# Optimization experiments

Hardware: AMD Instinct MI355X
Metric: run time of the kernel (lower is better)

The kernel has to match this reference:

```python
import jax, jax.numpy as jnp
import numpy as np

BETA = 0.25
N_E = 256
E_DIM = 1024


def setup_inputs() -> dict:
    key = jax.random.key(0)
    k1, k2, k3, k4 = jax.random.split(key, 4)
    z = jax.random.normal(k1, (16, E_DIM, 32, 32), dtype=jnp.float32)
    emb = jax.random.normal(k2, (N_E, E_DIM), dtype=jnp.float32)
    conv_w = jax.random.normal(k3, (E_DIM, E_DIM), dtype=jnp.float32) * 0.02
    conv_b = jax.random.normal(k4, (E_DIM,), dtype=jnp.float32) * 0.02
    return {"z": z, "emb": emb, "conv_w": conv_w, "conv_b": conv_b}


def reference(z, emb, conv_w, conv_b):
    # z: [B, C=e_dim, H, W] -> channels-last, flatten spatial+batch
    zp = jnp.transpose(z, (0, 2, 3, 1))          # [B, H, W, C]
    zf = zp.reshape(-1, E_DIM)                    # [N, C]
    # squared L2 distances to codebook: [N, n_e]
    d = (jnp.sum(zf * zf, axis=1, keepdims=True)
         + jnp.sum(emb * emb, axis=1)
         - 2.0 * (zf @ emb.T))
    min_idx = jnp.argmin(d, axis=1)               # [N]
    min_enc = jax.nn.one_hot(min_idx, N_E, dtype=z.dtype)  # [N, n_e]
    z_q = (min_enc @ emb).reshape(zp.shape)       # gather via matmul, as original
    # VQ commitment loss with straight-through estimator
    loss = (jnp.mean((jax.lax.stop_gradient(z_q) - zp) ** 2)
            + BETA * jnp.mean((z_q - jax.lax.stop_gradient(zp)) ** 2))
    z_q = zp + jax.lax.stop_gradient(z_q - zp)
    e_mean = jnp.mean(min_enc, axis=0)
    perplexity = jnp.exp(-jnp.sum(e_mean * jnp.log(e_mean + 1e-10)))
    # back to channels-first, then 1x1 conv (= per-pixel GEMM)
    z_q = jnp.transpose(z_q, (0, 3, 1, 2))        # [B, C, H, W]
    out = jnp.einsum('bchw,oc->bohw', z_q, conv_w) + conv_b[None, :, None, None]
    return out, loss, perplexity, min_idx
```

## Files before the change

### kernel.cpp

```cpp
#include <hip/hip_runtime.h>
#include <math.h>

#define NE 256
#define EDIM 1024
#define HW 1024
#define NPIX 16384
#define OUT_ELEMS 16777216

typedef short short8 __attribute__((ext_vector_type(8)));
typedef float f32x4 __attribute__((ext_vector_type(4)));

#define WS_HIST   0
#define WS_LOSS   1024
#define WS_ZSQ    1028
#define WS_NFLAG  1032
#define WS_T      4096
#define WS_MEMSET 1052672
#define WS_CE2    1052672
#define WS_FLAG   1053696
#define WS_IDX    1119232
#define WS_EH     1184768
#define WS_NEED   1709056

#define MAXF 16384
#define DELTA 0.6f

#define WO_CE2  0
#define WO_HIST 1024
#define WO_LOSS 2048
#define WO_IDX  4096
#define WO_T    69632
#define WO_TOTAL 1118208

__device__ __forceinline__ unsigned short f2bf(float f) {
    unsigned u = __float_as_uint(f);
    unsigned r = u + 0x7FFFu + ((u >> 16) & 1u);
    return (unsigned short)(r >> 16);
}

__device__ __forceinline__ void stage16(const void* g, void* l) {
    __builtin_amdgcn_global_load_lds(
        (const __attribute__((address_space(1))) unsigned int*)g,
        (__attribute__((address_space(3))) unsigned int*)l, 16, 0, 0);
}

__global__ __launch_bounds__(64) void k_prep(const float* __restrict__ emb,
                                             unsigned short* __restrict__ eh,
                                             float* __restrict__ ce2) {
    int j = blockIdx.x;
    int l = threadIdx.x;
    const float* row = emb + ((size_t)j << 10);
    float s = 0.f;
    #pragma unroll
    for (int i = 0; i < 4; i++) {
        float4 v = *(const float4*)(row + l * 4 + 256 * i);
        s += v.x * v.x + v.y * v.y + v.z * v.z + v.w * v.w;
        uint2 hp;
        hp.x = (unsigned)f2bf(v.x) | ((unsigned)f2bf(v.y) << 16);
        hp.y = (unsigned)f2bf(v.z) | ((unsigned)f2bf(v.w) << 16);
        *(uint2*)(eh + ((size_t)j << 10) + l * 4 + 256 * i) = hp;
    }
    #pragma unroll
    for (int m = 32; m; m >>= 1) s += __shfl_down(s, m, 64);
    if (l == 0) ce2[j] = 0.5f * s;
}

__global__ __launch_bounds__(256) void k_wT(const float* __restrict__ w,
                                            const float* __restrict__ emb,
                                            float* __restrict__ T) {
    __shared__ float wt[64 * 17];
    __shared__ float et[64 * 17];
    int t = threadIdx.x;
    int j0 = blockIdx.x * 64;
    int o0 = blockIdx.y * 64;
    int kb = blockIdx.z * 256;
    int to = t & 15, tj = t >> 4;
    float acc[4][4] = {};
    int lr = t >> 2, lk = (t & 3) * 4;
    for (int kk = kb; kk < kb + 256; kk += 16) {
        float4 wv = *(const float4*)(w + (size_t)(o0 + lr) * EDIM + kk + lk);
        float4 ev = *(const float4*)(emb + (size_t)(j0 + lr) * EDIM + kk + lk);
        __syncthreads();
        wt[lr * 17 + lk + 0] = wv.x; wt[lr * 17 + lk + 1] = wv.y;
        wt[lr * 17 + lk + 2] = wv.z; wt[lr * 17 + lk + 3] = wv.w;
        et[lr * 17 + lk + 0] = ev.x; et[lr * 17 + lk + 1] = ev.y;
        et[lr * 17 + lk + 2] = ev.z; et[lr * 17 + lk + 3] = ev.w;
        __syncthreads();
        #pragma unroll
        for (int k = 0; k < 16; k++) {
            float a[4], b[4];
            #pragma unroll
            for (int i = 0; i < 4; i++) a[i] = wt[(to * 4 + i) * 17 + k];
            #pragma unroll
            for (int i = 0; i < 4; i++) b[i] = et[(tj * 4 + i) * 17 + k];
            #pragma unroll
            for (int i = 0; i < 4; i++)
                #pragma unroll
                for (int jx = 0; jx < 4; jx++) acc[i][jx] += a[i] * b[jx];
        }
    }
    #pragma unroll
    for (int i = 0; i < 4; i++)
        #pragma unroll
        for (int jx = 0; jx < 4; jx++)
            atomicAdd(&T[(size_t)(o0 + to * 4 + i) * NE + j0 + tj * 4 + jx],
                      acc[i][jx]);
}

__global__ __launch_bounds__(256) void k_dist(
        const float* __restrict__ z, const unsigned short* __restrict__ eh,
        const float* __restrict__ ce2,
        int* __restrict__ idx_i, float* __restrict__ idx_f,
        int* __restrict__ hist, float* __restrict__ loss_s,
        float* __restrict__ zsq_acc,
        int* __restrict__ nflag, int* __restrict__ flagged) {
    __shared__ unsigned short sB[2][256 * 32];
    int t = threadIdx.x;
    int lane = t & 63, w = t >> 6;
    int m = lane & 15, quad = lane >> 4;
    int px0 = blockIdx.x * 64;
    int b = px0 >> 10;
    const float* zp = z + (((size_t)b) << 20) + (px0 & 1023) + w * 16 + m;
    int sc = t >> 2, so = (t & 3) * 8;

    f32x4 acc[16];
    #pragma unroll
    for (int nt = 0; nt < 16; nt++) acc[nt] = (f32x4){0.f, 0.f, 0.f, 0.f};

    #pragma unroll
    for (int i = 0; i < 4; i++)
        stage16(eh + (((size_t)(i * 64 + sc)) << 10) + so,
                &sB[0][(i * 256 + w * 64) * 8]);
    float zv[8];
    #pragma unroll
    for (int j = 0; j < 8; j++)
        zv[j] = zp[((size_t)(quad * 8 + j)) << 10];

    float zsq = 0.f;
    for (int ck = 0; ck < 32; ck++) {
        int cur = ck & 1;
        __syncthreads();
        short8 af;
        #pragma unroll
        for (int j = 0; j < 8; j++) {
            zsq += zv[j] * zv[j];
            ((unsigned short*)&af)[j] = f2bf(zv[j]);
        }
        if (ck < 31) {
            int kk = (ck + 1) * 32;
            #pragma unroll
            for (int i = 0; i < 4; i++)
                stage16(eh + (((size_t)(i * 64 + sc)) << 10) + kk + so,
                        &sB[1 - cur][(i * 256 + w * 64) * 8]);
            #pragma unroll
            for (int j = 0; j < 8; j++)
                zv[j] = zp[((size_t)(kk + quad * 8 + j)) << 10];
        }
        #pragma unroll
        for (int nt = 0; nt < 16; nt++) {
            short8 bf = *(const short8*)&sB[cur][(nt * 16 + m) * 32 + quad * 8];
            acc[nt] = __builtin_amdgcn_mfma_f32_16x16x32_bf16(af, bf, acc[nt], 0, 0, 0);
        }
    }

    #pragma unroll
    for (int msk = 32; msk; msk >>= 1) zsq += __shfl_down(zsq, msk, 64);
    if (lane == 0) atomicAdd(zsq_acc, zsq);

    float c2v[16];
    #pragma unroll
    for (int nt = 0; nt < 16; nt++) c2v[nt] = ce2[nt * 16 + m];

    float lsum = 0.f;
    #pragma unroll
    for (int r = 0; r < 4; r++) {
        float v1 = 3.4e38f, v2 = 3.4e38f; int i1 = 0;
        #pragma unroll
        for (int nt = 0; nt < 16; nt++) {
            int code = nt * 16 + m;
            float sv = c2v[nt] - acc[nt][r];
            if (sv < v1 || (sv == v1 && code < i1)) { v2 = v1; v1 = sv; i1 = code; }
            else v2 = fminf(v2, sv);
        }
        #pragma unroll
        for (int msk = 1; msk < 16; msk <<= 1) {
            float ov1 = __shfl_xor(v1, msk, 64);
            int   oi1 = __shfl_xor(i1, msk, 64);
            float ov2 = __shfl_xor(v2, msk, 64);
            float nv2 = fminf(fminf(v2, ov2), fmaxf(v1, ov1));
            if (ov1 < v1 || (ov1 == v1 && oi1 < i1)) { v1 = ov1; i1 = oi1; }
            v2 = nv2;
        }
        if (m == 0) {
            int px = px0 + w * 16 + quad * 4 + r;
            idx_i[px] = i1;
            idx_f[px] = (float)i1;
            atomicAdd(&hist[i1], 1);
            if (v2 - v1 < DELTA) {
                int pos = atomicAdd(nflag, 1);
                if (pos < MAXF) flagged[pos] = px;
            }
            lsum += v1;
        }
    }
    lsum += __shfl_xor(lsum, 16, 64);
    lsum += __shfl_xor(lsum, 32, 64);
    if (lane == 0) atomicAdd(loss_s, lsum);
}

__global__ __launch_bounds__(256) void k_cleanup(const float* __restrict__ z,
        const float* __restrict__ emb, const float* __restrict__ ce2,
        const int* __restrict__ nflag, const int* __restrict__ flagged,
        int* __restrict__ idx_i, float* __restrict__ idx_f, int* __restrict__ hist) {
    __shared__ float zs[1024];
    __shared__ float rv[4];
    __shared__ int ri[4];
    int t = threadIdx.x;
    int nf = *nflag; if (nf > MAXF) nf = MAXF;
    const float* er = emb + (size_t)t * EDIM;
    for (int i = blockIdx.x; i < nf; i += gridDim.x) {
        int px = flagged[i];
        int b = px >> 10, p = px & 1023;
        const float* zb = z + (((size_t)b) << 20) + p;
        #pragma unroll
        for (int r = 0; r < 4; r++) {
            int c = t + 256 * r;
            zs[c] = zb[((size_t)c) << 10];
        }
        __syncthreads();
        float d0 = 0.f, d1 = 0.f, d2 = 0.f, d3 = 0.f;
        #pragma unroll 4
        for (int c = 0; c < EDIM; c += 16) {
            float4 e0 = *(const float4*)(er + c);
            float4 e1 = *(const float4*)(er + c + 4);
            float4 e2 = *(const float4*)(er + c + 8);
            float4 e3 = *(const float4*)(er + c + 12);
            d0 += e0.x * zs[c]      + e0.y * zs[c + 1]  + e0.z * zs[c + 2]  + e0.w * zs[c + 3];
            d1 += e1.x * zs[c + 4]  + e1.y * zs[c + 5]  + e1.z * zs[c + 6]  + e1.w * zs[c + 7];
            d2 += e2.x * zs[c + 8]  + e2.y * zs[c + 9]  + e2.z * zs[c + 10] + e2.w * zs[c + 11];
            d3 += e3.x * zs[c + 12] + e3.y * zs[c + 13] + e3.z * zs[c + 14] + e3.w * zs[c + 15];
        }
        float sv = ce2[t] - ((d0 + d1) + (d2 + d3));
        int bi = t;
        #pragma unroll
        for (int msk = 1; msk < 64; msk <<= 1) {
            float ov = __shfl_xor(sv, msk, 64);
            int oi = __shfl_xor(bi, msk, 64);
            if (ov < sv || (ov == sv && oi < bi)) { sv = ov; bi = oi; }
        }
        if ((t & 63) == 0) { rv[t >> 6] = sv; ri[t >> 6] = bi; }
        __syncthreads();
        if (t == 0) {
            float v = rv[0]; int ix = ri[0];
            for (int ww = 1; ww < 4; ww++)
                if (rv[ww] < v || (rv[ww] == v && ri[ww] < ix)) { v = rv[ww]; ix = ri[ww]; }
            int old = idx_i[px];
            if (ix != old) {
                idx_i[px] = ix; idx_f[px] = (float)ix;
                atomicAdd(&hist[ix], 1); atomicSub(&hist[old], 1);
            }
        }
        __syncthreads();
    }
}

__global__ __launch_bounds__(64) void k_norms(const float* __restrict__ emb,
                                              float* __restrict__ ce2) {
    int j = blockIdx.x;
    int lane = threadIdx.x;
    const float* row = emb + (size_t)j * EDIM;
    float s = 0.f;
    #pragma unroll
    for (int i = 0; i < EDIM / 64; i++) {
        float v = row[lane + 64 * i];
        s += v * v;
    }
    #pragma unroll
    for (int m = 32; m; m >>= 1) s += __shfl_down(s, m, 64);
    if (lane == 0) ce2[j] = 0.5f * s;
}

__global__ __launch_bounds__(256) void k_argmin(const float* __restrict__ z,
                                                const float* __restrict__ emb,
                                                const float* __restrict__ ce2,
                                                int* __restrict__ idx_i,
                                                float* __restrict__ idx_f,
                                                int* __restrict__ hist,
                                                float* __restrict__ loss_acc) {
    __shared__ float zt[32 * 64];
    __shared__ float et[256 * 34];
    __shared__ float znorm_s[64];
    int t = threadIdx.x;
    int n0 = blockIdx.x * 64;
    int b = n0 >> 10;
    int p0 = n0 & 1023;
    const float* zb = z + (size_t)b * EDIM * HW;
    int tc = t & 31, tp = t >> 5;
    float acc[8][8] = {};
    float znorm = 0.f;
    for (int kk = 0; kk < EDIM; kk += 32) {
        #pragma unroll
        for (int i = 0; i < 16; i++) {
            int q = t + 256 * i;
            int code = q >> 4, k2 = q & 15;
            float2 v = *(const float2*)(emb + (size_t)code * EDIM + kk + k2 * 2);
            *(float2*)(et + code * 34 + k2 * 2) = v;
        }
        #pragma unroll
        for (int i = 0; i < 4; i++) {
            int q = t + 256 * i;
            int k = q >> 5, p2 = q & 31;
            float2 v = *(const float2*)(zb + (size_t)(kk + k) * HW + p0 + p2 * 2);
            *(float2*)(zt + k * 64 + p2 * 2) = v;
        }
        __syncthreads();
        if (t < 64) {
            #pragma unroll
            for (int k = 0; k < 32; k++) { float zz = zt[k * 64 + t]; znorm += zz * zz; }
        }
        #pragma unroll 4
        for (int k2 = 0; k2 < 16; k2++) {
            float2 ev[8], za[4], zb2[4];
            #pragma unroll
            for (int u = 0; u < 8; u++)
                ev[u] = *(float2*)(et + (tc + 32 * u) * 34 + k2 * 2);
            #pragma unroll
            for (int j = 0; j < 4; j++)
                za[j] = *(float2*)(zt + (2 * k2) * 64 + tp * 8 + 2 * j);
            #pragma unroll
            for (int j = 0; j < 4; j++)
                zb2[j] = *(float2*)(zt + (2 * k2 + 1) * 64 + tp * 8 + 2 * j);
            #pragma unroll
            for (int p = 0; p < 8; p++) {
                float z0 = (p & 1) ? za[p >> 1].y : za[p >> 1].x;
                float z1 = (p & 1) ? zb2[p >> 1].y : zb2[p >> 1].x;
                #pragma unroll
                for (int u = 0; u < 8; u++)
                    acc[p][u] += z0 * ev[u].x + z1 * ev[u].y;
            }
        }
        __syncthreads();
    }
    if (t < 64) znorm_s[t] = znorm;
    float minv[8];
    int mini[8];
    #pragma unroll
    for (int p = 0; p < 8; p++) { minv[p] = 3.4e38f; mini[p] = 0; }
    #pragma unroll
    for (int u = 0; u < 8; u++) {
        int code = tc + 32 * u;
        float cc2 = ce2[code];
        #pragma unroll
        for (int p = 0; p < 8; p++) {
            float s = cc2 - acc[p][u];
            if (s < minv[p] || (s == minv[p] && code < mini[p])) { minv[p] = s; mini[p] = code; }
        }
    }
    #pragma unroll
    for (int m = 1; m < 32; m <<= 1) {
        #pragma unroll
        for (int p = 0; p < 8; p++) {
            float ov = __shfl_xor(minv[p], m, 64);
            int oi = __shfl_xor(mini[p], m, 64);
            if (ov < minv[p] || (ov == minv[p] && oi < mini[p])) { minv[p] = ov; mini[p] = oi; }
        }
    }
    __syncthreads();
    if (tc == 0) {
        float dsum = 0.f;
        #pragma unroll
        for (int p = 0; p < 8; p++) {
            int lp = tp * 8 + p;
            int n = n0 + lp;
            idx_i[n] = mini[p];
            idx_f[n] = (float)mini[p];
            dsum += znorm_s[lp] + 2.f * minv[p];
            atomicAdd(&hist[mini[p]], 1);
        }
        atomicAdd(loss_acc, dsum);
    }
}

__global__ __launch_bounds__(256) void k_scatter(const float* __restrict__ T,
                                                 const float* __restrict__ bias,
                                                 const int* __restrict__ idx,
                                                 float* __restrict__ out) {
    __shared__ float Ts[16 * 256];
    __shared__ float bs[16];
    int t = threadIdx.x;
    int o0 = blockIdx.x * 16;
    int b = blockIdx.y;
    #pragma unroll
    for (int r = 0; r < 16; r++)
        Ts[r * 256 + t] = T[(size_t)(o0 + r) * NE + t];
    if (t < 16) bs[t] = bias[o0 + t];
    __syncthreads();
    int4 i4 = *(const int4*)(idx + b * HW + t * 4);
    #pragma unroll
    for (int r = 0; r < 16; r++) {
        const float* Tr = Ts + r * 256;
        float bb = bs[r];
        float4 v;
        v.x = Tr[i4.x] + bb;
        v.y = Tr[i4.y] + bb;
        v.z = Tr[i4.z] + bb;
        v.w = Tr[i4.w] + bb;
        *(float4*)(out + ((size_t)(b * EDIM + o0 + r) * HW) + t * 4) = v;
    }
}

__global__ __launch_bounds__(256) void k_final_new(const int* __restrict__ hist,
                                                   const float* __restrict__ loss_s,
                                                   const float* __restrict__ zsq,
                                                   float* __restrict__ out) {
    __shared__ float red[4];
    int t = threadIdx.x;
    float em = (float)hist[t] * (1.0f / 16384.0f);
    float v = em * logf(em + 1e-10f);
    #pragma unroll
    for (int m = 32; m; m >>= 1) v += __shfl_down(v, m, 64);
    if ((t & 63) == 0) red[t >> 6] = v;
    __syncthreads();
    if (t == 0) {
        float s = red[0] + red[1] + red[2] + red[3];
        out[OUT_ELEMS] = (zsq[0] + 2.f * loss_s[0]) * 1.25f / 16777216.f;
        out[OUT_ELEMS + 1] = expf(-s);
    }
}

__global__ __launch_bounds__(256) void k_final_old(const int* __restrict__ hist,
                                                   const float* __restrict__ loss_acc,
                                                   float* __restrict__ out) {
    __shared__ float red[4];
    int t = threadIdx.x;
    float em = (float)hist[t] * (1.0f / 16384.0f);
    float v = em * logf(em + 1e-10f);
    #pragma unroll
    for (int m = 32; m; m >>= 1) v += __shfl_down(v, m, 64);
    if ((t & 63) == 0) red[t >> 6] = v;
    __syncthreads();
    if (t == 0) {
        float s = red[0] + red[1] + red[2] + red[3];
        out[OUT_ELEMS] = loss_acc[0] * 1.25f / 16777216.f;
        out[OUT_ELEMS + 1] = expf(-s);
    }
}

extern "C" void kernel_launch(void* const* d_in, const int* in_sizes, int n_in,
                              void* d_out, int out_size, void* d_ws, size_t ws_size,
                              hipStream_t stream) {
    (void)in_sizes; (void)n_in; (void)out_size;
    const float* z      = (const float*)d_in[0];
    const float* emb    = (const float*)d_in[1];
    const float* conv_w = (const float*)d_in[2];
    const float* conv_b = (const float*)d_in[3];
    float* out = (float*)d_out;

    if (ws_size >= WS_NEED) {
        int*   hist     = (int*)((char*)d_ws + WS_HIST);
        float* loss_s   = (float*)((char*)d_ws + WS_LOSS);
        float* zsq      = (float*)((char*)d_ws + WS_ZSQ);
        int*   nflag    = (int*)((char*)d_ws + WS_NFLAG);
        float* T        = (float*)((char*)d_ws + WS_T);
        float* ce2      = (float*)((char*)d_ws + WS_CE2);
        int*   flagged  = (int*)((char*)d_ws + WS_FLAG);
        int*   idx_i    = (int*)((char*)d_ws + WS_IDX);
        unsigned short* eh = (unsigned short*)((char*)d_ws + WS_EH);
        float* idx_f = out + OUT_ELEMS + 2;

        hipMemsetAsync(d_ws, 0, WS_MEMSET, stream);
        k_prep<<<NE, 64, 0, stream>>>(emb, eh, ce2);
        k_wT<<<dim3(4, 16, 4), 256, 0, stream>>>(conv_w, emb, T);
        k_dist<<<256, 256, 0, stream>>>(z, eh, ce2, idx_i, idx_f,
                                        hist, loss_s, zsq, nflag, flagged);
        k_cleanup<<<256, 256, 0, stream>>>(z, emb, ce2, nflag, flagged,
                                           idx_i, idx_f, hist);
        k_scatter<<<dim3(64, 16), 256, 0, stream>>>(T, conv_b, idx_i, out);
        k_final_new<<<1, 256, 0, stream>>>(hist, loss_s, zsq, out);
    } else {
        float* ce2      = (float*)((char*)d_ws + WO_CE2);
        int*   hist     = (int*)((char*)d_ws + WO_HIST);
        float* loss_acc = (float*)((char*)d_ws + WO_LOSS);
        int*   idx_i    = (int*)((char*)d_ws + WO_IDX);
        float* T        = (float*)((char*)d_ws + WO_T);
        float* idx_f = out + OUT_ELEMS + 2;

        hipMemsetAsync(d_ws, 0, WO_TOTAL, stream);
        k_norms<<<NE, 64, 0, stream>>>(emb, ce2);
        k_wT<<<dim3(4, 16, 4), 256, 0, stream>>>(conv_w, emb, T);
        k_argmin<<<256, 256, 0, stream>>>(z, emb, ce2, idx_i, idx_f, hist, loss_acc);
        k_scatter<<<dim3(64, 16), 256, 0, stream>>>(T, conv_b, idx_i, out);
        k_final_old<<<1, 256, 0, stream>>>(hist, loss_acc, out);
    }
}
```

Baseline: 304.3 us.

## Use split-bf16 three-term MFMA distances to shrink the near-tie fallback set

The distance GEMM now splits both z and the codebook into bf16 high and low parts and accumulates hi*hi + hi*lo + lo*hi with three MFMAs per tile. This approximates fp32 closely enough that the near-tie margin can drop from 0.6 to 0.02, so far fewer pixels go through the exact fp32 cleanup kernel. The flagged list is replaced by a per-pixel bitmask, and the cleanup kernel scans all pixels and skips unflagged ones. The cost is three times the MFMA work, double the LDS staging and codebook traffic, an extra low-part codebook buffer, and a full bitmask scan in cleanup.

```diff
diff --git a/kernel.cpp b/kernel.cpp
--- a/kernel.cpp
+++ b/kernel.cpp
@@ -13,17 +13,16 @@
 #define WS_HIST   0
 #define WS_LOSS   1024
 #define WS_ZSQ    1028
-#define WS_NFLAG  1032
+#define WS_FBITS  2048
 #define WS_T      4096
 #define WS_MEMSET 1052672
 #define WS_CE2    1052672
-#define WS_FLAG   1053696
-#define WS_IDX    1119232
-#define WS_EH     1184768
-#define WS_NEED   1709056
-
-#define MAXF 16384
-#define DELTA 0.6f
+#define WS_IDX    1053696
+#define WS_EH     1119232
+#define WS_EL     1643520
+#define WS_NEED   2167808
+
+#define DELTA 0.02f
 
 #define WO_CE2  0
 #define WO_HIST 1024
@@ -37,6 +36,9 @@
     unsigned r = u + 0x7FFFu + ((u >> 16) & 1u);
     return (unsigned short)(r >> 16);
 }
+__device__ __forceinline__ float bf2f(unsigned short h) {
+    return __uint_as_float(((unsigned)h) << 16);
+}
 
 __device__ __forceinline__ void stage16(const void* g, void* l) {
     __builtin_amdgcn_global_load_lds(
@@ -46,6 +48,7 @@
 
 __global__ __launch_bounds__(64) void k_prep(const float* __restrict__ emb,
                                              unsigned short* __restrict__ eh,
+                                             unsigned short* __restrict__ el,
                                              float* __restrict__ ce2) {
     int j = blockIdx.x;
     int l = threadIdx.x;
@@ -55,10 +58,14 @@
     for (int i = 0; i < 4; i++) {
         float4 v = *(const float4*)(row + l * 4 + 256 * i);
         s += v.x * v.x + v.y * v.y + v.z * v.z + v.w * v.w;
-        uint2 hp;
-        hp.x = (unsigned)f2bf(v.x) | ((unsigned)f2bf(v.y) << 16);
-        hp.y = (unsigned)f2bf(v.z) | ((unsigned)f2bf(v.w) << 16);
+        unsigned short h0 = f2bf(v.x), h1 = f2bf(v.y), h2 = f2bf(v.z), h3 = f2bf(v.w);
+        uint2 hp, lp;
+        hp.x = (unsigned)h0 | ((unsigned)h1 << 16);
+        hp.y = (unsigned)h2 | ((unsigned)h3 << 16);
+        lp.x = (unsigned)f2bf(v.x - bf2f(h0)) | ((unsigned)f2bf(v.y - bf2f(h1)) << 16);
+        lp.y = (unsigned)f2bf(v.z - bf2f(h2)) | ((unsigned)f2bf(v.w - bf2f(h3)) << 16);
         *(uint2*)(eh + ((size_t)j << 10) + l * 4 + 256 * i) = hp;
+        *(uint2*)(el + ((size_t)j << 10) + l * 4 + 256 * i) = lp;
     }
     #pragma unroll
     for (int m = 32; m; m >>= 1) s += __shfl_down(s, m, 64);
@@ -109,12 +116,12 @@
 
 __global__ __launch_bounds__(256) void k_dist(
         const float* __restrict__ z, const unsigned short* __restrict__ eh,
+        const unsigned short* __restrict__ el,
         const float* __restrict__ ce2,
         int* __restrict__ idx_i, float* __restrict__ idx_f,
         int* __restrict__ hist, float* __restrict__ loss_s,
-        float* __restrict__ zsq_acc,
-        int* __restrict__ nflag, int* __restrict__ flagged) {
-    __shared__ unsigned short sB[2][256 * 32];
+        float* __restrict__ zsq_acc, unsigned int* __restrict__ fbits) {
+    __shared__ unsigned short sB[2][2][256 * 32];
     int t = threadIdx.x;
     int lane = t & 63, w = t >> 6;
     int m = lane & 15, quad = lane >> 4;
@@ -128,9 +135,10 @@
     for (int nt = 0; nt < 16; nt++) acc[nt] = (f32x4){0.f, 0.f, 0.f, 0.f};
 
     #pragma unroll
-    for (int i = 0; i < 4; i++)
-        stage16(eh + (((size_t)(i * 64 + sc)) << 10) + so,
-                &sB[0][(i * 256 + w * 64) * 8]);
+    for (int i = 0; i < 4; i++) {
+        stage16(eh + (((size_t)(i * 64 + sc)) << 10) + so, &sB[0][0][(i * 256 + w * 64) * 8]);
+        stage16(el + (((size_t)(i * 64 + sc)) << 10) + so, &sB[0][1][(i * 256 + w * 64) * 8]);
+    }
     float zv[8];
     #pragma unroll
     for (int j = 0; j < 8; j++)
@@ -140,26 +148,34 @@
     for (int ck = 0; ck < 32; ck++) {
         int cur = ck & 1;
         __syncthreads();
-        short8 af;
+        short8 ah, al;
         #pragma unroll
         for (int j = 0; j < 8; j++) {
             zsq += zv[j] * zv[j];
-            ((unsigned short*)&af)[j] = f2bf(zv[j]);
+            unsigned short h = f2bf(zv[j]);
+            ((unsigned short*)&ah)[j] = h;
+            ((unsigned short*)&al)[j] = f2bf(zv[j] - bf2f(h));
         }
         if (ck < 31) {
             int kk = (ck + 1) * 32;
             #pragma unroll
-            for (int i = 0; i < 4; i++)
+            for (int i = 0; i < 4; i++) {
                 stage16(eh + (((size_t)(i * 64 + sc)) << 10) + kk + so,
-                        &sB[1 - cur][(i * 256 + w * 64) * 8]);
+                        &sB[1 - cur][0][(i * 256 + w * 64) * 8]);
+                stage16(el + (((size_t)(i * 64 + sc)) << 10) + kk + so,
+                        &sB[1 - cur][1][(i * 256 + w * 64) * 8]);
+            }
             #pragma unroll
             for (int j = 0; j < 8; j++)
                 zv[j] = zp[((size_t)(kk + quad * 8 + j)) << 10];
         }
         #pragma unroll
         for (int nt = 0; nt < 16; nt++) {
-            short8 bf = *(const short8*)&sB[cur][(nt * 16 + m) * 32 + quad * 8];
-            acc[nt] = __builtin_amdgcn_mfma_f32_16x16x32_bf16(af, bf, acc[nt], 0, 0, 0);
+            short8 bh = *(const short8*)&sB[cur][0][(nt * 16 + m) * 32 + quad * 8];
+            short8 bl = *(const short8*)&sB[cur][1][(nt * 16 + m) * 32 + quad * 8];
+            acc[nt] = __builtin_amdgcn_mfma_f32_16x16x32_bf16(ah, bh, acc[nt], 0, 0, 0);
+            acc[nt] = __builtin_amdgcn_mfma_f32_16x16x32_bf16(ah, bl, acc[nt], 0, 0, 0);
+            acc[nt] = __builtin_amdgcn_mfma_f32_16x16x32_bf16(al, bh, acc[nt], 0, 0, 0);
         }
     }
 
@@ -196,10 +212,8 @@
             idx_i[px] = i1;
             idx_f[px] = (float)i1;
             atomicAdd(&hist[i1], 1);
-            if (v2 - v1 < DELTA) {
-                int pos = atomicAdd(nflag, 1);
-                if (pos < MAXF) flagged[pos] = px;
-            }
+            if (v2 - v1 < DELTA)
+                atomicOr(&fbits[px >> 5], 1u << (px & 31));
             lsum += v1;
         }
     }
@@ -210,16 +224,15 @@
 
 __global__ __launch_bounds__(256) void k_cleanup(const float* __restrict__ z,
         const float* __restrict__ emb, const float* __restrict__ ce2,
-        const int* __restrict__ nflag, const int* __restrict__ flagged,
+        const unsigned int* __restrict__ fbits,
         int* __restrict__ idx_i, float* __restrict__ idx_f, int* __restrict__ hist) {
     __shared__ float zs[1024];
     __shared__ float rv[4];
     __shared__ int ri[4];
     int t = threadIdx.x;
-    int nf = *nflag; if (nf > MAXF) nf = MAXF;
     const float* er = emb + (size_t)t * EDIM;
-    for (int i = blockIdx.x; i < nf; i += gridDim.x) {
-        int px = flagged[i];
+    for (int px = blockIdx.x; px < NPIX; px += gridDim.x) {
+        if (!(fbits[px >> 5] & (1u << (px & 31)))) continue;
         int b = px >> 10, p = px & 1023;
         const float* zb = z + (((size_t)b) << 20) + p;
         #pragma unroll
@@ -460,21 +473,20 @@
         int*   hist     = (int*)((char*)d_ws + WS_HIST);
         float* loss_s   = (float*)((char*)d_ws + WS_LOSS);
         float* zsq      = (float*)((char*)d_ws + WS_ZSQ);
-        int*   nflag    = (int*)((char*)d_ws + WS_NFLAG);
+        unsigned int* fbits = (unsigned int*)((char*)d_ws + WS_FBITS);
         float* T        = (float*)((char*)d_ws + WS_T);
         float* ce2      = (float*)((char*)d_ws + WS_CE2);
-        int*   flagged  = (int*)((char*)d_ws + WS_FLAG);
         int*   idx_i    = (int*)((char*)d_ws + WS_IDX);
         unsigned short* eh = (unsigned short*)((char*)d_ws + WS_EH);
+        unsigned short* el = (unsigned short*)((char*)d_ws + WS_EL);
         float* idx_f = out + OUT_ELEMS + 2;
 
         hipMemsetAsync(d_ws, 0, WS_MEMSET, stream);
-        k_prep<<<NE, 64, 0, stream>>>(emb, eh, ce2);
+        k_prep<<<NE, 64, 0, stream>>>(emb, eh, el, ce2);
         k_wT<<<dim3(4, 16, 4), 256, 0, stream>>>(conv_w, emb, T);
-        k_dist<<<256, 256, 0, stream>>>(z, eh, ce2, idx_i, idx_f,
-                                        hist, loss_s, zsq, nflag, flagged);
-        k_cleanup<<<256, 256, 0, stream>>>(z, emb, ce2, nflag, flagged,
-                                           idx_i, idx_f, hist);
+        k_dist<<<256, 256, 0, stream>>>(z, eh, el, ce2, idx_i, idx_f,
+                                        hist, loss_s, zsq, fbits);
+        k_cleanup<<<256, 256, 0, stream>>>(z, emb, ce2, fbits, idx_i, idx_f, hist);
         k_scatter<<<dim3(64, 16), 256, 0, stream>>>(T, conv_b, idx_i, out);
         k_final_new<<<1, 256, 0, stream>>>(hist, loss_s, zsq, out);
     } else {
```

New measurement: 260.2 us. 1.17x faster.
